# Optimization experiments

Measured on AMD Instinct MI355X. Metric: run time of the kernel, lower is better.

## Reference

```python
import jax, jax.numpy as jnp
import numpy as np

N_HEADS = 8

def gcn_conv(x, edge_index, W, b):
    # PyG GCNConv: add self-loops, symmetric normalization, linear transform + bias
    N = x.shape[0]
    loop = jnp.arange(N)
    src = jnp.concatenate([edge_index[0], loop])
    dst = jnp.concatenate([edge_index[1], loop])
    deg = jax.ops.segment_sum(jnp.ones(src.shape[0], dtype=x.dtype), dst, num_segments=N)
    dinv = jax.lax.rsqrt(jnp.maximum(deg, 1.0))  # deg >= 1 due to self-loops
    norm = dinv[src] * dinv[dst]                 # [E+N]
    h = x @ W                                    # [N, out]
    msg = h[src] * norm[:, None]                 # gather + scale
    return jax.ops.segment_sum(msg, dst, num_segments=N) + b

def layer_norm(x, g, b):
    mu = jnp.mean(x, axis=-1, keepdims=True)
    var = jnp.mean((x - mu) ** 2, axis=-1, keepdims=True)
    return (x - mu) * jax.lax.rsqrt(var + 1e-5) * g + b

def mha(q, kv, Wq, Wk, Wv, Wo):
    B, M, d = q.shape
    dh = d // N_HEADS
    Q = (q @ Wq).reshape(B, M, N_HEADS, dh)
    K = (kv @ Wk).reshape(B, kv.shape[1], N_HEADS, dh)
    V = (kv @ Wv).reshape(B, kv.shape[1], N_HEADS, dh)
    scale = jnp.asarray(1.0 / np.sqrt(dh), q.dtype)
    scores = jnp.einsum('bqhd,bkhd->bhqk', Q, K) * scale
    attn = jax.nn.softmax(scores, axis=-1)
    out = jnp.einsum('bhqk,bkhd->bqhd', attn, V).reshape(B, M, d)
    return out @ Wo

def setup_inputs() -> dict:
    key = jax.random.key(0)
    ks = jax.random.split(key, 24)
    B, M, d, dff, L = 32, 1024, 128, 512, 2
    N, E = B * M, 524288
    s = 0.02
    inp = {
        'enc_out_vari': jax.random.normal(ks[0], (B, M, d), jnp.float32),
        'x_enc': jax.random.normal(ks[1], (B, M, d), jnp.float32),
        'x_raw': jax.random.normal(ks[2], (N, d), jnp.float32),
        'edge_index': jax.random.randint(ks[3], (2, E), 0, N, jnp.int64 if jax.config.jax_enable_x64 else jnp.int32),
        'W_gcn1': s * jax.random.normal(ks[4], (d, d), jnp.float32),
        'b_gcn1': jnp.zeros((d,), jnp.float32),
        'W_gcn2': s * jax.random.normal(ks[5], (d, d), jnp.float32),
        'b_gcn2': jnp.zeros((d,), jnp.float32),
        'Wq': s * jax.random.normal(ks[6], (L, d, d), jnp.float32),
        'Wk': s * jax.random.normal(ks[7], (L, d, d), jnp.float32),
        'Wv': s * jax.random.normal(ks[8], (L, d, d), jnp.float32),
        'Wo': s * jax.random.normal(ks[9], (L, d, d), jnp.float32),
        'Wff1': s * jax.random.normal(ks[10], (L, d, dff), jnp.float32),
        'bff1': jnp.zeros((L, dff), jnp.float32),
        'Wff2': s * jax.random.normal(ks[11], (L, dff, d), jnp.float32),
        'bff2': jnp.zeros((L, d), jnp.float32),
        'ln1_g': jnp.ones((L, d), jnp.float32),
        'ln1_b': jnp.zeros((L, d), jnp.float32),
        'ln2_g': jnp.ones((L, d), jnp.float32),
        'ln2_b': jnp.zeros((L, d), jnp.float32),
    }
    return inp

def reference(enc_out_vari, x_enc, x_raw, edge_index, W_gcn1, b_gcn1, W_gcn2, b_gcn2,
              Wq, Wk, Wv, Wo, Wff1, bff1, Wff2, bff2, ln1_g, ln1_b, ln2_g, ln2_b):
    B, M, d = enc_out_vari.shape
    # GCN stack (dropout is identity in eval mode)
    x1 = jax.nn.relu(gcn_conv(x_raw, edge_index, W_gcn1, b_gcn1))
    x2 = jax.nn.relu(gcn_conv(x1, edge_index, W_gcn2, b_gcn2))
    x = x2.reshape(B, M, d)
    # Transformer encoder: cross-attention from enc_out_vari onto GCN features
    y = enc_out_vari
    L = Wq.shape[0]
    for l in range(L):
        a = mha(y, x, Wq[l], Wk[l], Wv[l], Wo[l])
        y = layer_norm(y + a, ln1_g[l], ln1_b[l])
        f = jax.nn.relu(y @ Wff1[l] + bff1[l]) @ Wff2[l] + bff2[l]
        y = layer_norm(y + f, ln2_g[l], ln2_b[l])
    return y
```

## Files before the change

kernel.cpp:

```cpp
#include <hip/hip_runtime.h>
#include <math.h>


typedef __attribute__((ext_vector_type(8)))  short short8;
typedef __attribute__((ext_vector_type(4)))  float f32x4;
typedef __attribute__((ext_vector_type(16))) float f32x16;

__device__ __forceinline__ unsigned short f2bf(float x) {
    unsigned u = __builtin_bit_cast(unsigned, x);
    u = (u + 0x7FFFu + ((u >> 16) & 1u)) >> 16;
    return (unsigned short)u;
}
__device__ __forceinline__ float bflo(unsigned u) { return __builtin_bit_cast(float, u << 16); }
__device__ __forceinline__ float bfhi(unsigned u) { return __builtin_bit_cast(float, u & 0xffff0000u); }
__device__ __forceinline__ float fast_exp2(float x) {
    float r; asm("v_exp_f32 %0, %1" : "=v"(r) : "v"(x)); return r;
}

__global__ void count_kernel(const int* __restrict__ dst, int* __restrict__ cnt, int E) {
    int e = blockIdx.x * 256 + threadIdx.x;
    if (e < E) atomicAdd(&cnt[dst[e]], 1);
}

__global__ __launch_bounds__(256)
void scanA_kernel(const int* __restrict__ cnt, int* __restrict__ partial)
{
    __shared__ int wsum[4];
    int t = threadIdx.x;
    int v = cnt[blockIdx.x * 256 + t];
    #pragma unroll
    for (int off = 32; off; off >>= 1) v += __shfl_xor(v, off, 64);
    if ((t & 63) == 0) wsum[t >> 6] = v;
    __syncthreads();
    if (t == 0) partial[blockIdx.x] = wsum[0] + wsum[1] + wsum[2] + wsum[3];
}

__global__ __launch_bounds__(256)
void scanC_kernel(const int* __restrict__ cnt, const int* __restrict__ partial,
                  int* __restrict__ off, int* __restrict__ cursor,
                  float* __restrict__ dinv, int N, int E)
{
    __shared__ int p[256];
    __shared__ int bsum[4];
    int t = threadIdx.x, b = blockIdx.x;
    int pv = (t < b) ? partial[t] : 0;
    #pragma unroll
    for (int o = 32; o; o >>= 1) pv += __shfl_xor(pv, o, 64);
    if ((t & 63) == 0) bsum[t >> 6] = pv;
    __syncthreads();
    const int base = bsum[0] + bsum[1] + bsum[2] + bsum[3];
    int i = b * 256 + t;
    int c = cnt[i];
    p[t] = c;
    __syncthreads();
    for (int o = 1; o < 256; o <<= 1) {
        int q = (t >= o) ? p[t - o] : 0;
        __syncthreads();
        p[t] += q;
        __syncthreads();
    }
    int ex = base + p[t] - c;
    off[i] = ex;
    cursor[i] = ex;
    dinv[i] = rsqrtf((float)c + 1.0f);
    if (b == 0 && t == 0) off[N] = E;
}

__global__ void place_kernel(const int* __restrict__ src, const int* __restrict__ dst,
                             int* __restrict__ cursor, int* __restrict__ csr_src, int E)
{
    int e = blockIdx.x * 256 + threadIdx.x;
    if (e < E) {
        int p = atomicAdd(&cursor[dst[e]], 1);
        csr_src[p] = src[e];
    }
}

__global__ __launch_bounds__(256)
void prep_kernel(const float* __restrict__ xraw, unsigned short* __restrict__ xrawh,
                 const float* __restrict__ enc, float* __restrict__ bufY,
                 unsigned short* __restrict__ bufYh,
                 const float* Wg1, const float* Wg2, const float* Wq, const float* Wk,
                 const float* Wv, const float* Wo, const float* Wff1, const float* Wff2,
                 unsigned short* __restrict__ out, int nconv)
{
    const int bid = blockIdx.x, tid = threadIdx.x;
    if (bid < nconv) {
        int i = bid * 256 + tid;
        float4 v = ((const float4*)xraw)[i];
        ushort4 h; h.x = f2bf(v.x); h.y = f2bf(v.y); h.z = f2bf(v.z); h.w = f2bf(v.w);
        ((ushort4*)xrawh)[i] = h;
        return;
    }
    if (bid < 2 * nconv) {
        int i = (bid - nconv) * 256 + tid;
        float4 v = ((const float4*)enc)[i];
        ((float4*)bufY)[i] = v;
        ushort4 h; h.x = f2bf(v.x); h.y = f2bf(v.y); h.z = f2bf(v.z); h.w = f2bf(v.w);
        ((ushort4*)bufYh)[i] = h;
        return;
    }
    const int bid2 = bid - 2 * nconv;
    const int slot = bid2 >> 8;
    const int bx   = bid2 & 255;
    const float* src; int ks; int Ns; size_t doff; float scale = 1.0f;
    if      (slot == 0)  { src = Wg1;                        ks = 7; Ns = 128; doff = 0; }
    else if (slot == 1)  { src = Wg2;                        ks = 7; Ns = 128; doff = 16384; }
    else if (slot <= 3)  { src = Wq  + (slot - 2)  * 16384;  ks = 7; Ns = 128; doff = 32768  + (size_t)(slot - 2)  * 16384; scale = 0.36067376022f; }
    else if (slot <= 5)  { src = Wk  + (slot - 4)  * 16384;  ks = 7; Ns = 128; doff = 65536  + (size_t)(slot - 4)  * 32768; }
    else if (slot <= 7)  { src = Wv  + (slot - 6)  * 16384;  ks = 7; Ns = 128; doff = 65536  + (size_t)(slot - 6)  * 32768 + 16384; }
    else if (slot <= 9)  { src = Wo  + (slot - 8)  * 16384;  ks = 7; Ns = 128; doff = 131072 + (size_t)(slot - 8)  * 16384; }
    else if (slot <= 11) { src = Wff1 + (slot - 10) * 65536; ks = 7; Ns = 512; doff = 163840 + (size_t)(slot - 10) * 65536; }
    else                 { src = Wff2 + (slot - 12) * 65536; ks = 9; Ns = 128; doff = 294912 + (size_t)(slot - 12) * 65536; }
    const int total = Ns << ks;
    int id = bx * 256 + tid;
    if (id >= total) return;
    int n = id >> ks;
    int k = id & ((1 << ks) - 1);
    out[doff + id] = f2bf(src[(size_t)k * Ns + n] * scale);
}

__device__ __forceinline__
void gemm64_body(unsigned short* As, unsigned short* Ws,
                 const unsigned short* __restrict__ A,
                 const unsigned short* __restrict__ Wt,
                 void* __restrict__ C, void* __restrict__ C2, int K, int ldc,
                 const float* __restrict__ bias, const float* __restrict__ rowscale,
                 int relu, int mode, int bx, int by)
{
    const int tid  = threadIdx.x;
    const int lane = tid & 63, wave = tid >> 6;
    const int m31 = lane & 31, hi = lane >> 5;
    const int row0 = bx * 64;
    const int c0   = by * 64;
    const int wrow = (wave & 1) * 32;
    const int wcol = (wave >> 1) * 32;
    const int sr = tid >> 2, sk = (tid & 3) * 16;

    f32x16 acc = {};

    for (int kt = 0; kt < K; kt += 64) {
        if (kt) __syncthreads();
        *(short8*)&As[sr * 72 + sk]     = *(const short8*)&A [(size_t)(row0 + sr) * K + kt + sk];
        *(short8*)&As[sr * 72 + sk + 8] = *(const short8*)&A [(size_t)(row0 + sr) * K + kt + sk + 8];
        *(short8*)&Ws[sr * 72 + sk]     = *(const short8*)&Wt[(size_t)(c0   + sr) * K + kt + sk];
        *(short8*)&Ws[sr * 72 + sk + 8] = *(const short8*)&Wt[(size_t)(c0   + sr) * K + kt + sk + 8];
        __syncthreads();
        #pragma unroll
        for (int ks = 0; ks < 4; ++ks) {
            short8 af = *(const short8*)&As[(wrow + m31) * 72 + ks * 16 + hi * 8];
            short8 bf = *(const short8*)&Ws[(wcol + m31) * 72 + ks * 16 + hi * 8];
            acc = __builtin_amdgcn_mfma_f32_32x32x16_bf16(af, bf, acc, 0, 0, 0);
        }
    }

    const int col = c0 + wcol + m31;
    #pragma unroll
    for (int r = 0; r < 16; ++r) {
        const int row = row0 + wrow + (r & 3) + 8 * (r >> 2) + 4 * hi;
        float v = acc[r];
        if (rowscale) v *= rowscale[row];
        if (bias) v += bias[col];
        if (relu) v = fmaxf(v, 0.0f);
        if (mode == 1) {
            ((unsigned short*)C)[(size_t)row * ldc + col] = f2bf(v);
        } else {
            if (col < 128) {
                ((unsigned short*)C)[(size_t)row * 128 + col] = f2bf(v);
            } else {
                int ch = col - 128, hh = ch >> 4, dd = ch & 15;
                int kg = row & 1023;
                int w  = kg & 127;
                int slot = ((w >> 5) << 5) | (((w >> 2) & 3) << 3)
                         | (((w >> 4) & 1) << 2) | (w & 3);
                int kpos = (kg & ~127) | slot;
                ((unsigned short*)C2)[(((size_t)(row >> 10) * 8 + hh) * 16 + dd) * 1024
                                      + kpos] = f2bf(v);
            }
        }
    }
}

__global__ __launch_bounds__(256)
void gemm64_kernel(const unsigned short* __restrict__ A,
                   const unsigned short* __restrict__ Wt,
                   void* __restrict__ C, void* __restrict__ C2, int K,
                   const float* __restrict__ bias, const float* __restrict__ rowscale,
                   int relu, int mode)
{
    __shared__ unsigned short As[64 * 72];
    __shared__ unsigned short Ws[64 * 72];
    gemm64_body(As, Ws, A, Wt, C, C2, K, gridDim.y * 64, bias, rowscale, relu, mode,
                blockIdx.x, blockIdx.y);
}

__global__ __launch_bounds__(256)
void qkv_kernel(const unsigned short* __restrict__ Yh, const unsigned short* __restrict__ wtq,
                unsigned short* __restrict__ Qh,
                const unsigned short* __restrict__ Bh, const unsigned short* __restrict__ wtkv,
                unsigned short* __restrict__ Kg, unsigned short* __restrict__ Vtg)
{
    __shared__ unsigned short As[64 * 72];
    __shared__ unsigned short Ws[64 * 72];
    if (blockIdx.y < 2)
        gemm64_body(As, Ws, Yh, wtq, Qh, nullptr, 128, 128, nullptr, nullptr, 0, 1,
                    blockIdx.x, blockIdx.y);
    else
        gemm64_body(As, Ws, Bh, wtkv, Kg, Vtg, 128, 256, nullptr, nullptr, 0, 2,
                    blockIdx.x, blockIdx.y - 2);
}

__global__ __launch_bounds__(256)
void gemm_ln_kernel(const unsigned short* __restrict__ A,
                    const unsigned short* __restrict__ Wt, int K,
                    const float* __restrict__ bias,
                    const float* __restrict__ resid_in, float* __restrict__ resid_out,
                    unsigned short* __restrict__ yh,
                    const float* __restrict__ lng, const float* __restrict__ lnb)
{
    __shared__ __align__(16) unsigned char smraw[23040];
    unsigned short* As = (unsigned short*)smraw;
    unsigned short* Ws = (unsigned short*)(smraw + 4608);

    const int tid  = threadIdx.x;
    const int lane = tid & 63, wave = tid >> 6;
    const int m31 = lane & 31, hi = lane >> 5;
    const int row0 = blockIdx.x * 32;
    const int wcol = wave * 32;
    const int sr = tid >> 3, sk = (tid & 7) * 8;
    const int wr = tid >> 1, wo = (tid & 1) * 32;

    const unsigned short* Ap = &A [(size_t)(row0 + sr) * K + sk];
    const unsigned short* Wp = &Wt[(size_t)wr * K + wo];

    short8 ra0 = *(const short8*)(Ap);
    short8 rw0 = *(const short8*)(Wp);
    short8 rw1 = *(const short8*)(Wp + 8);
    short8 rw2 = *(const short8*)(Wp + 16);
    short8 rw3 = *(const short8*)(Wp + 24);

    f32x16 acc = {};

    for (int kt = 0; kt < K; kt += 64) {
        *(short8*)&As[sr * 72 + sk]      = ra0;
        *(short8*)&Ws[wr * 72 + wo]      = rw0;
        *(short8*)&Ws[wr * 72 + wo + 8]  = rw1;
        *(short8*)&Ws[wr * 72 + wo + 16] = rw2;
        *(short8*)&Ws[wr * 72 + wo + 24] = rw3;
        if (kt + 64 < K) {
            ra0 = *(const short8*)(Ap + kt + 64);
            rw0 = *(const short8*)(Wp + kt + 64);
            rw1 = *(const short8*)(Wp + kt + 72);
            rw2 = *(const short8*)(Wp + kt + 80);
            rw3 = *(const short8*)(Wp + kt + 88);
        }
        __syncthreads();
        #pragma unroll
        for (int ks = 0; ks < 4; ++ks) {
            short8 af = *(const short8*)&As[m31 * 72 + ks * 16 + hi * 8];
            short8 bf = *(const short8*)&Ws[(wcol + m31) * 72 + ks * 16 + hi * 8];
            acc = __builtin_amdgcn_mfma_f32_32x32x16_bf16(af, bf, acc, 0, 0, 0);
        }
        __syncthreads();
    }

    float* Ts = (float*)smraw;
    {
        const int col = wcol + m31;
        #pragma unroll
        for (int r = 0; r < 16; ++r) {
            const int rl = (r & 3) + 8 * (r >> 2) + 4 * hi;
            float v = acc[r];
            if (bias) v += bias[col];
            Ts[rl * 130 + col] = v;
        }
    }
    __syncthreads();
    const int r  = tid >> 3;
    const int cq = tid & 7;
    const int row = row0 + r;
    float v[16], s1 = 0.f, s2 = 0.f;
    const float* yr = resid_in + (size_t)row * 128 + cq * 16;
    #pragma unroll
    for (int i = 0; i < 4; ++i) {
        float4 yv = *(const float4*)&yr[i * 4];
        float ys[4] = {yv.x, yv.y, yv.z, yv.w};
        #pragma unroll
        for (int j = 0; j < 4; ++j) {
            float t = Ts[r * 130 + cq * 16 + i * 4 + j] + ys[j];
            v[i * 4 + j] = t; s1 += t; s2 += t * t;
        }
    }
    s1 += __shfl_xor(s1, 1, 64); s1 += __shfl_xor(s1, 2, 64); s1 += __shfl_xor(s1, 4, 64);
    s2 += __shfl_xor(s2, 1, 64); s2 += __shfl_xor(s2, 2, 64); s2 += __shfl_xor(s2, 4, 64);
    const float mu  = s1 * (1.0f / 128.0f);
    const float inv = rsqrtf(s2 * (1.0f / 128.0f) - mu * mu + 1e-5f);
    float* outr = resid_out + (size_t)row * 128 + cq * 16;
    unsigned short* yhr = yh + (size_t)row * 128 + cq * 16;
    #pragma unroll
    for (int i = 0; i < 4; ++i) {
        float o0 = (v[i*4+0] - mu) * inv * lng[cq*16 + i*4 + 0] + lnb[cq*16 + i*4 + 0];
        float o1 = (v[i*4+1] - mu) * inv * lng[cq*16 + i*4 + 1] + lnb[cq*16 + i*4 + 1];
        float o2 = (v[i*4+2] - mu) * inv * lng[cq*16 + i*4 + 2] + lnb[cq*16 + i*4 + 2];
        float o3 = (v[i*4+3] - mu) * inv * lng[cq*16 + i*4 + 3] + lnb[cq*16 + i*4 + 3];
        float4 ov; ov.x = o0; ov.y = o1; ov.z = o2; ov.w = o3;
        *(float4*)&outr[i * 4] = ov;
        ushort4 hv; hv.x = f2bf(o0); hv.y = f2bf(o1); hv.z = f2bf(o2); hv.w = f2bf(o3);
        *(ushort4*)&yhr[i * 4] = hv;
    }
}

__global__ __launch_bounds__(256)
void gather_kernel(const unsigned short* __restrict__ hs, const int* __restrict__ csr_off,
                   const int* __restrict__ csr_src, const float* __restrict__ dinv,
                   const float* __restrict__ bias, unsigned short* __restrict__ out, int N)
{
    const int node = blockIdx.x * 4 + (threadIdx.x >> 6);
    const int lane = threadIdx.x & 63;
    const int s0 = __builtin_amdgcn_readfirstlane(csr_off[node]);
    const int s1 = __builtin_amdgcn_readfirstlane(csr_off[node + 1]);
    const unsigned* hsu = (const unsigned*)hs;

    unsigned u = hsu[(size_t)node * 64 + lane];
    float a0 = bflo(u), a1 = bfhi(u);

    int j = s0;
    for (; j + 4 <= s1; j += 4) {
        int i0 = csr_src[j];
        int i1 = csr_src[j + 1];
        int i2 = csr_src[j + 2];
        int i3 = csr_src[j + 3];
        unsigned uA = hsu[(size_t)i0 * 64 + lane];
        unsigned uB = hsu[(size_t)i1 * 64 + lane];
        unsigned uC = hsu[(size_t)i2 * 64 + lane];
        unsigned uD = hsu[(size_t)i3 * 64 + lane];
        a0 += (bflo(uA) + bflo(uB)) + (bflo(uC) + bflo(uD));
        a1 += (bfhi(uA) + bfhi(uB)) + (bfhi(uC) + bfhi(uD));
    }
    for (; j < s1; ++j) {
        int ib = csr_src[j];
        unsigned ub = hsu[(size_t)ib * 64 + lane];
        a0 += bflo(ub); a1 += bfhi(ub);
    }
    float di = dinv[node];
    float v0 = fmaxf(a0 * di + bias[lane * 2],     0.0f);
    float v1 = fmaxf(a1 * di + bias[lane * 2 + 1], 0.0f);
    ((unsigned*)out)[(size_t)node * 64 + lane] =
        ((unsigned)f2bf(v1) << 16) | (unsigned)f2bf(v0);
}

__global__ __launch_bounds__(256)
void attn_mfma_kernel(const unsigned short* __restrict__ Qh,
                      const unsigned short* __restrict__ Kg,
                      const unsigned short* __restrict__ Vtg,
                      unsigned short* __restrict__ Obh)
{
    __shared__ __align__(16) unsigned short Ks[128 * 16];
    __shared__ __align__(16) unsigned short Vt[16 * 136];

    const int tid  = threadIdx.x;
    const int lane = tid & 63, wave = tid >> 6;
    const int quad = lane >> 4, l16 = lane & 15;
    const int q0 = blockIdx.x * 64, h = blockIdx.y, b = blockIdx.z;

    const int key  = tid >> 1, half = (tid & 1) * 8;
    const int dim  = tid >> 4, kc = (tid & 15) * 8;
    const unsigned short* Kp = &Kg[((size_t)b * 1024 + key) * 128 + h * 16 + half];
    const unsigned short* Vp = &Vtg[(((size_t)b * 8 + h) * 16 + dim) * 1024 + kc];

    short8 qa = {};
    if (quad < 2) {
        qa = *(const short8*)&Qh[((size_t)b * 1024 + q0 + wave * 16 + l16) * 128 + h * 16 + quad * 8];
    }

    const short one_bf = (short)0x3F80;
    const short8 onesv = {one_bf, one_bf, one_bf, one_bf,
                          one_bf, one_bf, one_bf, one_bf};

    f32x4 o    = {0.f, 0.f, 0.f, 0.f};
    f32x4 lacc = {0.f, 0.f, 0.f, 0.f};
    const int kread = (quad & 1) * 8;

    short8 kreg = *(const short8*)(Kp);
    short8 vreg = *(const short8*)(Vp);

    for (int it = 0; it < 8; ++it) {
        *(short8*)&Ks[key * 16 + half] = kreg;
        *(short8*)&Vt[dim * 136 + kc]  = vreg;
        if (it < 7) {
            kreg = *(const short8*)(Kp + (size_t)(it + 1) * 128 * 128);
            vreg = *(const short8*)(Vp + (it + 1) * 128);
        }
        __syncthreads();

        f32x4 s[8];
        f32x4 zc = {0.f, 0.f, 0.f, 0.f};
        #pragma unroll
        for (int g = 0; g < 8; ++g) {
            short8 kb = *(const short8*)&Ks[(g * 16 + l16) * 16 + kread];
            s[g] = __builtin_amdgcn_mfma_f32_16x16x32_bf16(kb, qa, zc, 0, 0, 0);
        }

        #pragma unroll
        for (int t = 0; t < 4; ++t) {
            float p00 = fast_exp2(s[2*t][0]);
            float p01 = fast_exp2(s[2*t][1]);
            float p02 = fast_exp2(s[2*t][2]);
            float p03 = fast_exp2(s[2*t][3]);
            float p10 = fast_exp2(s[2*t+1][0]);
            float p11 = fast_exp2(s[2*t+1][1]);
            float p12 = fast_exp2(s[2*t+1][2]);
            float p13 = fast_exp2(s[2*t+1][3]);
            uint4 pk;
            pk.x = __builtin_amdgcn_perm(__builtin_bit_cast(unsigned, p01),
                                         __builtin_bit_cast(unsigned, p00), 0x07060302u);
            pk.y = __builtin_amdgcn_perm(__builtin_bit_cast(unsigned, p03),
                                         __builtin_bit_cast(unsigned, p02), 0x07060302u);
            pk.z = __builtin_amdgcn_perm(__builtin_bit_cast(unsigned, p11),
                                         __builtin_bit_cast(unsigned, p10), 0x07060302u);
            pk.w = __builtin_amdgcn_perm(__builtin_bit_cast(unsigned, p13),
                                         __builtin_bit_cast(unsigned, p12), 0x07060302u);
            short8 pa = __builtin_bit_cast(short8, pk);
            short8 vb = *(const short8*)&Vt[l16 * 136 + t * 32 + quad * 8];
            o    = __builtin_amdgcn_mfma_f32_16x16x32_bf16(pa, vb, o, 0, 0, 0);
            lacc = __builtin_amdgcn_mfma_f32_16x16x32_bf16(pa, onesv, lacc, 0, 0, 0);
        }
        if (it < 7) __syncthreads();
    }

    #pragma unroll
    for (int r = 0; r < 4; ++r) {
        float linv = 1.0f / lacc[r];
        int qrow = q0 + wave * 16 + quad * 4 + r;
        Obh[((size_t)b * 1024 + qrow) * 128 + h * 16 + l16] = f2bf(o[r] * linv);
    }
}

extern "C" void kernel_launch(void* const* d_in, const int* in_sizes, int n_in,
                              void* d_out, int out_size, void* d_ws, size_t ws_size,
                              hipStream_t stream)
{
    const float* enc  = (const float*)d_in[0];
    const float* xraw = (const float*)d_in[2];
    const int*   ei   = (const int*)d_in[3];
    const float* Wg1  = (const float*)d_in[4];
    const float* bg1  = (const float*)d_in[5];
    const float* Wg2  = (const float*)d_in[6];
    const float* bg2  = (const float*)d_in[7];
    const float* Wq   = (const float*)d_in[8];
    const float* Wk   = (const float*)d_in[9];
    const float* Wv   = (const float*)d_in[10];
    const float* Wo   = (const float*)d_in[11];
    const float* Wff1 = (const float*)d_in[12];
    const float* bff1 = (const float*)d_in[13];
    const float* Wff2 = (const float*)d_in[14];
    const float* bff2 = (const float*)d_in[15];
    const float* ln1g = (const float*)d_in[16];
    const float* ln1b = (const float*)d_in[17];
    const float* ln2g = (const float*)d_in[18];
    const float* ln2b = (const float*)d_in[19];

    const int E  = in_sizes[3] / 2;
    const int N  = in_sizes[2] / 128;
    const int BM = in_sizes[0] / 128;
    const int B  = BM / 1024;
    const int L  = in_sizes[8] / (128 * 128);

    const int* srcE = ei;
    const int* dstE = ei + E;

    const size_t ND = (size_t)N * 128;

    float* ws   = (float*)d_ws;
    float* dinv = ws;
    int* cnt     = (int*)(ws + 32768);
    int* csr_off = cnt + N;
    int* cursor  = csr_off + N + 4;
    int* csr_src = cursor + N;
    int* partial = csr_src + E;
    int* pbase   = partial + 128;
    float* bufY  = (float*)(((uintptr_t)(pbase + 128) + 255) & ~(uintptr_t)255);
    unsigned short* ush   = (unsigned short*)(bufY + ND);
    unsigned short* bufYh = ush;
    unsigned short* bufBh = bufYh + ND;
    unsigned short* region = bufBh + ND;
    unsigned short* Qh  = region;
    unsigned short* Kg  = region + ND;
    unsigned short* Vtg = region + 2 * ND;
    unsigned short* Th  = region + 3 * ND;
    unsigned short* Hh  = region;
    unsigned short* hsh   = region;
    unsigned short* xrawh = region + ND;
    unsigned short* wt  = region + 4 * ND;

    hipMemsetAsync(cnt, 0, (size_t)N * sizeof(int), stream);
    count_kernel<<<(E + 255) / 256, 256, 0, stream>>>(dstE, cnt, E);
    scanA_kernel<<<N / 256, 256, 0, stream>>>(cnt, partial);
    scanC_kernel<<<N / 256, 256, 0, stream>>>(cnt, partial, csr_off, cursor, dinv, N, E);
    place_kernel<<<(E + 255) / 256, 256, 0, stream>>>(srcE, dstE, cursor, csr_src, E);

    const int nconv = (int)(ND / 1024);
    prep_kernel<<<2 * nconv + 14 * 256, 256, 0, stream>>>(
        xraw, xrawh, enc, bufY, bufYh,
        Wg1, Wg2, Wq, Wk, Wv, Wo, Wff1, Wff2, wt, nconv);

    gemm64_kernel<<<dim3(N / 64, 2), 256, 0, stream>>>(xrawh, wt, hsh, nullptr, 128,
        nullptr, dinv, 0, 1);
    gather_kernel<<<N / 4, 256, 0, stream>>>(hsh, csr_off, csr_src, dinv, bg1, bufBh, N);
    gemm64_kernel<<<dim3(N / 64, 2), 256, 0, stream>>>(bufBh, wt + 16384, hsh, nullptr, 128,
        nullptr, dinv, 0, 1);
    gather_kernel<<<N / 4, 256, 0, stream>>>(hsh, csr_off, csr_src, dinv, bg2, bufBh, N);

    for (int l = 0; l < L; ++l) {
        const unsigned short* wtq  = wt + 32768  + (size_t)l * 16384;
        const unsigned short* wtkv = wt + 65536  + (size_t)l * 32768;
        const unsigned short* wto  = wt + 131072 + (size_t)l * 16384;
        const unsigned short* wtf1 = wt + 163840 + (size_t)l * 65536;
        const unsigned short* wtf2 = wt + 294912 + (size_t)l * 65536;

        qkv_kernel<<<dim3(BM / 64, 6), 256, 0, stream>>>(bufYh, wtq, Qh,
                                                         bufBh, wtkv, Kg, Vtg);

        attn_mfma_kernel<<<dim3(16, 8, B), 256, 0, stream>>>(Qh, Kg, Vtg, Th);

        gemm_ln_kernel<<<BM / 32, 256, 0, stream>>>(Th, wto, 128, nullptr,
            bufY, bufY, bufYh, ln1g + l * 128, ln1b + l * 128);

        gemm64_kernel<<<dim3(BM / 64, 8), 256, 0, stream>>>(bufYh, wtf1, Hh, nullptr, 128,
            bff1 + l * 512, nullptr, 1, 1);

        float* rout = (l == L - 1) ? (float*)d_out : bufY;
        gemm_ln_kernel<<<BM / 32, 256, 0, stream>>>(Hh, wtf2, 512, bff2 + l * 128,
            bufY, rout, bufYh, ln2g + l * 128, ln2b + l * 128);
    }
}
```

Measured before the change: 481.1 us.

## Keep residual stream in bf16 only and double-buffer attention K/V tiles

```diff
diff --git a/kernel.cpp b/kernel.cpp
--- a/kernel.cpp
+++ b/kernel.cpp
@@ -78,26 +78,19 @@
 
 __global__ __launch_bounds__(256)
 void prep_kernel(const float* __restrict__ xraw, unsigned short* __restrict__ xrawh,
-                 const float* __restrict__ enc, float* __restrict__ bufY,
-                 unsigned short* __restrict__ bufYh,
+                 const float* __restrict__ enc, unsigned short* __restrict__ bufYh,
                  const float* Wg1, const float* Wg2, const float* Wq, const float* Wk,
                  const float* Wv, const float* Wo, const float* Wff1, const float* Wff2,
                  unsigned short* __restrict__ out, int nconv)
 {
     const int bid = blockIdx.x, tid = threadIdx.x;
-    if (bid < nconv) {
-        int i = bid * 256 + tid;
-        float4 v = ((const float4*)xraw)[i];
+    if (bid < 2 * nconv) {
+        const float* s = (bid < nconv) ? xraw : enc;
+        unsigned short* d = (bid < nconv) ? xrawh : bufYh;
+        int i = ((bid < nconv) ? bid : bid - nconv) * 256 + tid;
+        float4 v = ((const float4*)s)[i];
         ushort4 h; h.x = f2bf(v.x); h.y = f2bf(v.y); h.z = f2bf(v.z); h.w = f2bf(v.w);
-        ((ushort4*)xrawh)[i] = h;
-        return;
-    }
-    if (bid < 2 * nconv) {
-        int i = (bid - nconv) * 256 + tid;
-        float4 v = ((const float4*)enc)[i];
-        ((float4*)bufY)[i] = v;
-        ushort4 h; h.x = f2bf(v.x); h.y = f2bf(v.y); h.z = f2bf(v.z); h.w = f2bf(v.w);
-        ((ushort4*)bufYh)[i] = h;
+        ((ushort4*)d)[i] = h;
         return;
     }
     const int bid2 = bid - 2 * nconv;
@@ -214,7 +207,8 @@
 void gemm_ln_kernel(const unsigned short* __restrict__ A,
                     const unsigned short* __restrict__ Wt, int K,
                     const float* __restrict__ bias,
-                    const float* __restrict__ resid_in, float* __restrict__ resid_out,
+                    const unsigned short* __restrict__ resid_in,
+                    float* __restrict__ fout,
                     unsigned short* __restrict__ yh,
                     const float* __restrict__ lng, const float* __restrict__ lnb)
 {
@@ -280,11 +274,11 @@
     const int cq = tid & 7;
     const int row = row0 + r;
     float v[16], s1 = 0.f, s2 = 0.f;
-    const float* yr = resid_in + (size_t)row * 128 + cq * 16;
+    const unsigned short* yr = resid_in + (size_t)row * 128 + cq * 16;
     #pragma unroll
     for (int i = 0; i < 4; ++i) {
-        float4 yv = *(const float4*)&yr[i * 4];
-        float ys[4] = {yv.x, yv.y, yv.z, yv.w};
+        uint2 yv = *(const uint2*)&yr[i * 4];
+        float ys[4] = {bflo(yv.x), bfhi(yv.x), bflo(yv.y), bfhi(yv.y)};
         #pragma unroll
         for (int j = 0; j < 4; ++j) {
             float t = Ts[r * 130 + cq * 16 + i * 4 + j] + ys[j];
@@ -295,7 +289,6 @@
     s2 += __shfl_xor(s2, 1, 64); s2 += __shfl_xor(s2, 2, 64); s2 += __shfl_xor(s2, 4, 64);
     const float mu  = s1 * (1.0f / 128.0f);
     const float inv = rsqrtf(s2 * (1.0f / 128.0f) - mu * mu + 1e-5f);
-    float* outr = resid_out + (size_t)row * 128 + cq * 16;
     unsigned short* yhr = yh + (size_t)row * 128 + cq * 16;
     #pragma unroll
     for (int i = 0; i < 4; ++i) {
@@ -303,8 +296,10 @@
         float o1 = (v[i*4+1] - mu) * inv * lng[cq*16 + i*4 + 1] + lnb[cq*16 + i*4 + 1];
         float o2 = (v[i*4+2] - mu) * inv * lng[cq*16 + i*4 + 2] + lnb[cq*16 + i*4 + 2];
         float o3 = (v[i*4+3] - mu) * inv * lng[cq*16 + i*4 + 3] + lnb[cq*16 + i*4 + 3];
-        float4 ov; ov.x = o0; ov.y = o1; ov.z = o2; ov.w = o3;
-        *(float4*)&outr[i * 4] = ov;
+        if (fout) {
+            float4 ov; ov.x = o0; ov.y = o1; ov.z = o2; ov.w = o3;
+            *(float4*)&fout[(size_t)row * 128 + cq * 16 + i * 4] = ov;
+        }
         ushort4 hv; hv.x = f2bf(o0); hv.y = f2bf(o1); hv.z = f2bf(o2); hv.w = f2bf(o3);
         *(ushort4*)&yhr[i * 4] = hv;
     }
@@ -355,8 +350,8 @@
                       const unsigned short* __restrict__ Vtg,
                       unsigned short* __restrict__ Obh)
 {
-    __shared__ __align__(16) unsigned short Ks[128 * 16];
-    __shared__ __align__(16) unsigned short Vt[16 * 136];
+    __shared__ __align__(16) unsigned short Ks[2][128 * 16];
+    __shared__ __align__(16) unsigned short Vt[2][16 * 136];
 
     const int tid  = threadIdx.x;
     const int lane = tid & 63, wave = tid >> 6;
@@ -383,21 +378,20 @@
 
     short8 kreg = *(const short8*)(Kp);
     short8 vreg = *(const short8*)(Vp);
+    *(short8*)&Ks[0][key * 16 + half] = kreg;
+    *(short8*)&Vt[0][dim * 136 + kc]  = vreg;
+    kreg = *(const short8*)(Kp + (size_t)128 * 128);
+    vreg = *(const short8*)(Vp + 128);
+    __syncthreads();
 
     for (int it = 0; it < 8; ++it) {
-        *(short8*)&Ks[key * 16 + half] = kreg;
-        *(short8*)&Vt[dim * 136 + kc]  = vreg;
-        if (it < 7) {
-            kreg = *(const short8*)(Kp + (size_t)(it + 1) * 128 * 128);
-            vreg = *(const short8*)(Vp + (it + 1) * 128);
-        }
-        __syncthreads();
+        const int cur = it & 1;
 
         f32x4 s[8];
         f32x4 zc = {0.f, 0.f, 0.f, 0.f};
         #pragma unroll
         for (int g = 0; g < 8; ++g) {
-            short8 kb = *(const short8*)&Ks[(g * 16 + l16) * 16 + kread];
+            short8 kb = *(const short8*)&Ks[cur][(g * 16 + l16) * 16 + kread];
             s[g] = __builtin_amdgcn_mfma_f32_16x16x32_bf16(kb, qa, zc, 0, 0, 0);
         }
 
@@ -421,11 +415,20 @@
             pk.w = __builtin_amdgcn_perm(__builtin_bit_cast(unsigned, p13),
                                          __builtin_bit_cast(unsigned, p12), 0x07060302u);
             short8 pa = __builtin_bit_cast(short8, pk);
-            short8 vb = *(const short8*)&Vt[l16 * 136 + t * 32 + quad * 8];
+            short8 vb = *(const short8*)&Vt[cur][l16 * 136 + t * 32 + quad * 8];
             o    = __builtin_amdgcn_mfma_f32_16x16x32_bf16(pa, vb, o, 0, 0, 0);
             lacc = __builtin_amdgcn_mfma_f32_16x16x32_bf16(pa, onesv, lacc, 0, 0, 0);
         }
-        if (it < 7) __syncthreads();
+
+        if (it < 7) {
+            *(short8*)&Ks[cur ^ 1][key * 16 + half] = kreg;
+            *(short8*)&Vt[cur ^ 1][dim * 136 + kc]  = vreg;
+            if (it < 6) {
+                kreg = *(const short8*)(Kp + (size_t)(it + 2) * 128 * 128);
+                vreg = *(const short8*)(Vp + (it + 2) * 128);
+            }
+            __syncthreads();
+        }
     }
 
     #pragma unroll
@@ -479,9 +482,8 @@
     int* csr_src = cursor + N;
     int* partial = csr_src + E;
     int* pbase   = partial + 128;
-    float* bufY  = (float*)(((uintptr_t)(pbase + 128) + 255) & ~(uintptr_t)255);
-    unsigned short* ush   = (unsigned short*)(bufY + ND);
-    unsigned short* bufYh = ush;
+    unsigned short* bufYh =
+        (unsigned short*)(((uintptr_t)(pbase + 128) + 255) & ~(uintptr_t)255);
     unsigned short* bufBh = bufYh + ND;
     unsigned short* region = bufBh + ND;
     unsigned short* Qh  = region;
@@ -501,7 +503,7 @@
 
     const int nconv = (int)(ND / 1024);
     prep_kernel<<<2 * nconv + 14 * 256, 256, 0, stream>>>(
-        xraw, xrawh, enc, bufY, bufYh,
+        xraw, xrawh, enc, bufYh,
         Wg1, Wg2, Wq, Wk, Wv, Wo, Wff1, Wff2, wt, nconv);
 
     gemm64_kernel<<<dim3(N / 64, 2), 256, 0, stream>>>(xrawh, wt, hsh, nullptr, 128,
@@ -524,13 +526,13 @@
         attn_mfma_kernel<<<dim3(16, 8, B), 256, 0, stream>>>(Qh, Kg, Vtg, Th);
 
         gemm_ln_kernel<<<BM / 32, 256, 0, stream>>>(Th, wto, 128, nullptr,
-            bufY, bufY, bufYh, ln1g + l * 128, ln1b + l * 128);
+            bufYh, nullptr, bufYh, ln1g + l * 128, ln1b + l * 128);
 
         gemm64_kernel<<<dim3(BM / 64, 8), 256, 0, stream>>>(bufYh, wtf1, Hh, nullptr, 128,
             bff1 + l * 512, nullptr, 1, 1);
 
-        float* rout = (l == L - 1) ? (float*)d_out : bufY;
+        float* rout = (l == L - 1) ? (float*)d_out : nullptr;
         gemm_ln_kernel<<<BM / 32, 256, 0, stream>>>(Hh, wtf2, 512, bff2 + l * 128,
-            bufY, rout, bufYh, ln2g + l * 128, ln2b + l * 128);
-    }
-}
+            bufYh, rout, bufYh, ln2g + l * 128, ln2b + l * 128);
+    }
+}
```

Measured after the change: 464.5 us. 3.4% less time.
